# Optimization experiments

Measured on AMD Instinct MI355X. Metric: run time of the kernel, lower is better.

The kernel has to match this reference:

```python
import jax, jax.numpy as jnp
import numpy as np

SIGMA = 1.0
ALPHA = 1.5
EPS = 1e-08
N, D = 8192, 128


def setup_inputs() -> dict:
    key = jax.random.key(0)
    k1, k2 = jax.random.split(key)
    z1 = jax.random.normal(k1, (N, D), dtype=jnp.float32)
    z2 = jax.random.normal(k2, (N, D), dtype=jnp.float32)
    return {"z1": z1, "z2": z2}


def _l2_normalize(x, eps=1e-12):
    # matches F.normalize(x, dim=1): x / max(||x||, eps)
    n = jnp.linalg.norm(x, axis=1, keepdims=True)
    return x / jnp.maximum(n, eps)


def _f_prime(u):
    # KL divergence: f'(u) = log(u + eps) + 1
    return jnp.log(u + EPS) + 1.0


def _f_star(t):
    # KL divergence conjugate: f*(t) = exp(t - 1)
    return jnp.exp(t - 1.0)


def reference(z1, z2):
    z1 = _l2_normalize(z1)
    z2 = _l2_normalize(z2)
    n = z1.shape[0]

    # positive term: ||z1_i - z2_i||^2 per row
    d_pos = jnp.sum((z1 - z2) ** 2, axis=1)                       # (N,)
    g_pos = jnp.exp(-d_pos / (2.0 * SIGMA ** 2))
    s_pos = _f_prime(g_pos)

    # negative term: squared pairwise distances within z1 (N x N)
    sq = jnp.sum(z1 * z1, axis=1)                                  # (N,)
    d2 = sq[:, None] + sq[None, :] - 2.0 * (z1 @ z1.T)             # (N, N)
    d2 = jnp.maximum(d2, 0.0)
    g_neg = jnp.exp(-d2 / (2.0 * SIGMA ** 2))
    s_neg = _f_prime(g_neg)
    star_neg = _f_star(s_neg)

    # masked mean over off-diagonal entries (N*(N-1) of them)
    off_diag = 1.0 - jnp.eye(n, dtype=star_neg.dtype)
    star_mean = jnp.sum(star_neg * off_diag) / (n * (n - 1))

    loss = -jnp.mean(s_pos) + ALPHA * star_mean
    return loss
```

## Files before the change

kernel.cpp:

```cpp
#include <hip/hip_runtime.h>

#define NROWS 8192
#define DIM 128
#define NT 64
#define NBLK 512

typedef _Float16 f16x8 __attribute__((ext_vector_type(8)));
typedef _Float16 f16x2 __attribute__((ext_vector_type(2)));
typedef float f32x16 __attribute__((ext_vector_type(16)));

#define L2E 1.4426950408889634f

#define AS1(p) ((const __attribute__((address_space(1))) void*)(p))
#define AS3(p) ((__attribute__((address_space(3))) void*)(p))

__global__ __launch_bounds__(1024) void fmicl_normalize(
    const float* __restrict__ z1, const float* __restrict__ z2,
    _Float16* __restrict__ zh, float* __restrict__ sposB) {
  const int wid = threadIdx.x >> 6;
  const int lane = threadIdx.x & 63;
  const int row = blockIdx.x * 16 + wid;
  const float2 a = ((const float2*)(z1 + (size_t)row * DIM))[lane];
  const float2 b = ((const float2*)(z2 + (size_t)row * DIM))[lane];
  float s1 = a.x * a.x + a.y * a.y;
  float s2 = b.x * b.x + b.y * b.y;
#pragma unroll
  for (int off = 32; off; off >>= 1) {
    s1 += __shfl_xor(s1, off);
    s2 += __shfl_xor(s2, off);
  }
  const float inv1 = 1.0f / fmaxf(sqrtf(s1), 1e-12f);
  const float inv2 = 1.0f / fmaxf(sqrtf(s2), 1e-12f);
  const float n1x = a.x * inv1, n1y = a.y * inv1;
  const float n2x = b.x * inv2, n2y = b.y * inv2;
  const float dx = n1x - n2x, dy = n1y - n2y;
  float dp = dx * dx + dy * dy;
#pragma unroll
  for (int off = 32; off; off >>= 1) dp += __shfl_xor(dp, off);
  f16x2 h;
  h.x = (_Float16)n1x;
  h.y = (_Float16)n1y;
  *(f16x2*)(zh + (size_t)row * DIM + 2 * lane) = h;
  __shared__ float sposL[16];
  if (lane == 0)
    sposL[wid] = logf(expf(-0.5f * dp) + 1e-8f) + 1.0f;
  __syncthreads();
  if (threadIdx.x == 0) {
    float s = 0.0f;
#pragma unroll
    for (int k = 0; k < 16; ++k) s += sposL[k];
    sposB[blockIdx.x] = s;
  }
}

__device__ __forceinline__ void stageB(const _Float16* __restrict__ zh,
                                       _Float16* buf, int ct, int wid,
                                       int lane) {
  const _Float16* base = zh + ((size_t)ct << 7) * DIM;
#pragma unroll
  for (int it = 0; it < 4; ++it) {
    const int P = it * 8 + wid;
    const int R = P * 4 + (lane >> 4);
    const int cs = (lane & 15) ^ (R & 15);
    __builtin_amdgcn_global_load_lds(AS1(base + (size_t)R * DIM + cs * 8),
                                     AS3(buf + P * 512), 16, 0, 0);
  }
}

__global__ __launch_bounds__(512, 4) void fmicl_pairwise(
    const _Float16* __restrict__ zh, float* __restrict__ pairP) {
  __shared__ _Float16 B0[128 * DIM];
  __shared__ _Float16 B1[128 * DIM];
  __shared__ float wsum[8];

  const int tid = threadIdx.x;
  const int lane = tid & 63;
  const int wid = tid >> 6;
  const int l31 = lane & 31;
  const int lhi = lane >> 5;
  const int m = wid >> 1;
  const int n = wid & 1;

  const int c = (blockIdx.x & 7) * 64 + (blockIdx.x >> 3);
  const int nx = (c + 15) >> 4;
  const int base = 4 * c + nx;
  const int len = 4 + ((c & 15) == 0 ? 1 : 0);

  int rt = (int)(64.5f - sqrtf(64.5f * 64.5f - 2.0f * (float)base));
  if (rt < 0) rt = 0;
  while (rt > 0 && (rt * NT - (rt * (rt - 1)) / 2) > base) --rt;
  while (((rt + 1) * NT - ((rt + 1) * rt) / 2) <= base) ++rt;
  int ctt = rt + (base - (rt * NT - (rt * (rt - 1)) / 2));
  int rtt = rt;

  stageB(zh, B0, ctt, wid, lane);

  uint4 areg[8];
  int cur_rt = -1;
  float gsum = 0.0f;

#pragma unroll 1
  for (int t = 0; t < len; ++t) {
    if (rtt != cur_rt) {
      cur_rt = rtt;
      const uint4* ar =
          (const uint4*)(zh + (size_t)((rtt << 7) + m * 32 + l31) * DIM);
#pragma unroll
      for (int ks = 0; ks < 8; ++ks) areg[ks] = ar[2 * ks + lhi];
    }
    int nrt = rtt, nct = ctt + 1;
    if (nct == NT) { ++nrt; nct = nrt; }
    if (t + 1 < len) {
      stageB(zh, (t & 1) ? B0 : B1, nct, wid, lane);
      asm volatile("s_waitcnt vmcnt(4)" ::: "memory");
    } else {
      asm volatile("s_waitcnt vmcnt(0)" ::: "memory");
    }
    __builtin_amdgcn_s_barrier();
    __builtin_amdgcn_sched_barrier(0);

    const uint4* B4 = (const uint4*)((t & 1) ? B1 : B0);
    const int rb0 = n * 64 + l31;
    const int rb1 = n * 64 + 32 + l31;
    f32x16 acc0 = {}, acc1 = {};
#pragma unroll
    for (int ks = 0; ks < 8; ++ks) {
      const int kg = 2 * ks + lhi;
      const uint4 vb0 = B4[rb0 * 16 + (kg ^ (rb0 & 15))];
      const uint4 vb1 = B4[rb1 * 16 + (kg ^ (rb1 & 15))];
      const f16x8 af = __builtin_bit_cast(f16x8, areg[ks]);
      acc0 = __builtin_amdgcn_mfma_f32_32x32x16_f16(
          af, __builtin_bit_cast(f16x8, vb0), acc0, 0, 0, 0);
      acc1 = __builtin_amdgcn_mfma_f32_32x32x16_f16(
          af, __builtin_bit_cast(f16x8, vb1), acc1, 0, 0, 0);
    }

    float tsum = 0.0f;
    {
      const bool dsub = (rtt == ctt) && (m == 2 * n);
      if (dsub) {
#pragma unroll
        for (int r = 0; r < 16; ++r) {
          const float e = __builtin_amdgcn_exp2f(fmaf(L2E, acc0[r], -L2E));
          const int mloc = (r & 3) + 4 * lhi + 8 * (r >> 2);
          tsum += (mloc != l31) ? e : 0.0f;
        }
      } else {
#pragma unroll
        for (int r = 0; r < 16; ++r)
          tsum += __builtin_amdgcn_exp2f(fmaf(L2E, acc0[r], -L2E));
      }
    }
    {
      const bool dsub = (rtt == ctt) && (m == 2 * n + 1);
      if (dsub) {
#pragma unroll
        for (int r = 0; r < 16; ++r) {
          const float e = __builtin_amdgcn_exp2f(fmaf(L2E, acc1[r], -L2E));
          const int mloc = (r & 3) + 4 * lhi + 8 * (r >> 2);
          tsum += (mloc != l31) ? e : 0.0f;
        }
      } else {
#pragma unroll
        for (int r = 0; r < 16; ++r)
          tsum += __builtin_amdgcn_exp2f(fmaf(L2E, acc1[r], -L2E));
      }
    }
    gsum += (rtt == ctt) ? tsum : (tsum + tsum);

    __builtin_amdgcn_s_barrier();
    rtt = nrt;
    ctt = nct;
  }

#pragma unroll
  for (int off = 32; off; off >>= 1) gsum += __shfl_xor(gsum, off);
  if (lane == 0) wsum[wid] = gsum;
  __syncthreads();
  if (tid == 0) {
    float s = 0.0f;
#pragma unroll
    for (int q = 0; q < 8; ++q) s += wsum[q];
    pairP[c] = s;
  }
}

__global__ void fmicl_reduce(const float* __restrict__ pairP,
                             const float* __restrict__ sposB,
                             float* __restrict__ out) {
  const int t = threadIdx.x;
  double nsum = (t < NBLK) ? (double)pairP[t] : 0.0;
  double psum = (t < 512) ? (double)sposB[t] : 0.0;
#pragma unroll
  for (int off = 32; off; off >>= 1) {
    nsum += __shfl_xor(nsum, off);
    psum += __shfl_xor(psum, off);
  }
  __shared__ double ls[2][16];
  const int lane = t & 63;
  const int wid = t >> 6;
  if (lane == 0) {
    ls[0][wid] = nsum;
    ls[1][wid] = psum;
  }
  __syncthreads();
  if (t == 0) {
    double nn = 0.0, pp = 0.0;
#pragma unroll
    for (int q = 0; q < 16; ++q) {
      nn += ls[0][q];
      pp += ls[1][q];
    }
    const double pos_mean = pp / (double)NROWS;
    const double star_mean = nn / ((double)NROWS * (double)(NROWS - 1)) + 1e-8;
    out[0] = (float)(-pos_mean + 1.5 * star_mean);
  }
}

extern "C" void kernel_launch(void* const* d_in, const int* in_sizes, int n_in,
                              void* d_out, int out_size, void* d_ws,
                              size_t ws_size, hipStream_t stream) {
  const float* z1 = (const float*)d_in[0];
  const float* z2 = (const float*)d_in[1];
  float* out = (float*)d_out;
  char* ws = (char*)d_ws;

  float* pairP = (float*)(ws + 0);
  float* sposB = (float*)(ws + 4096);
  _Float16* zh = (_Float16*)(ws + 6144);

  fmicl_normalize<<<512, 1024, 0, stream>>>(z1, z2, zh, sposB);
  fmicl_pairwise<<<NBLK, 512, 0, stream>>>(zh, pairP);
  fmicl_reduce<<<1, 1024, 0, stream>>>(pairP, sposB, out);
}
```

Before: 30.00 us.

## Prefetch all B tiles into four LDS buffers and remap warps to 2x4 grid

New measurement: 42.60 us. 1.42x slower.

```diff
diff --git a/kernel.cpp b/kernel.cpp
--- a/kernel.cpp
+++ b/kernel.cpp
@@ -67,10 +67,73 @@
   }
 }
 
-__global__ __launch_bounds__(512, 4) void fmicl_pairwise(
+__device__ __forceinline__ void loadA(const _Float16* __restrict__ zh, int rt,
+                                      int mw, int l31, int lhi, uint4* a0,
+                                      uint4* a1) {
+  const uint4* r0 = (const uint4*)(zh + (size_t)((rt << 7) + mw * 64 + l31) * DIM);
+  const uint4* r1 = r0 + 32 * (DIM / 8);
+#pragma unroll
+  for (int ks = 0; ks < 8; ++ks) {
+    a0[ks] = r0[2 * ks + lhi];
+    a1[ks] = r1[2 * ks + lhi];
+  }
+}
+
+__device__ __forceinline__ void computeTile(const _Float16* __restrict__ buf,
+                                            int rtt, int ctt, int mw, int nw,
+                                            int l31, int lhi,
+                                            const uint4* a0, const uint4* a1,
+                                            float& gsum) {
+  const uint4* B4 = (const uint4*)buf;
+  const int rb = nw * 32 + l31;
+  f32x16 acc0 = {}, acc1 = {};
+#pragma unroll
+  for (int ks = 0; ks < 8; ++ks) {
+    const int kg = 2 * ks + lhi;
+    const uint4 vb = B4[rb * 16 + (kg ^ (rb & 15))];
+    const f16x8 bf = __builtin_bit_cast(f16x8, vb);
+    acc0 = __builtin_amdgcn_mfma_f32_32x32x16_f16(
+        __builtin_bit_cast(f16x8, a0[ks]), bf, acc0, 0, 0, 0);
+    acc1 = __builtin_amdgcn_mfma_f32_32x32x16_f16(
+        __builtin_bit_cast(f16x8, a1[ks]), bf, acc1, 0, 0, 0);
+  }
+  float tsum = 0.0f;
+  {
+    const bool dsub = (rtt == ctt) && (nw == 2 * mw);
+    if (dsub) {
+#pragma unroll
+      for (int r = 0; r < 16; ++r) {
+        const float e = __builtin_amdgcn_exp2f(fmaf(L2E, acc0[r], -L2E));
+        const int mloc = (r & 3) + 4 * lhi + 8 * (r >> 2);
+        tsum += (mloc != l31) ? e : 0.0f;
+      }
+    } else {
+#pragma unroll
+      for (int r = 0; r < 16; ++r)
+        tsum += __builtin_amdgcn_exp2f(fmaf(L2E, acc0[r], -L2E));
+    }
+  }
+  {
+    const bool dsub = (rtt == ctt) && (nw == 2 * mw + 1);
+    if (dsub) {
+#pragma unroll
+      for (int r = 0; r < 16; ++r) {
+        const float e = __builtin_amdgcn_exp2f(fmaf(L2E, acc1[r], -L2E));
+        const int mloc = (r & 3) + 4 * lhi + 8 * (r >> 2);
+        tsum += (mloc != l31) ? e : 0.0f;
+      }
+    } else {
+#pragma unroll
+      for (int r = 0; r < 16; ++r)
+        tsum += __builtin_amdgcn_exp2f(fmaf(L2E, acc1[r], -L2E));
+    }
+  }
+  gsum += (rtt == ctt) ? tsum : (tsum + tsum);
+}
+
+__global__ __launch_bounds__(512, 2) void fmicl_pairwise(
     const _Float16* __restrict__ zh, float* __restrict__ pairP) {
-  __shared__ _Float16 B0[128 * DIM];
-  __shared__ _Float16 B1[128 * DIM];
+  __shared__ _Float16 S[4][128 * DIM];
   __shared__ float wsum[8];
 
   const int tid = threadIdx.x;
@@ -78,99 +141,78 @@
   const int wid = tid >> 6;
   const int l31 = lane & 31;
   const int lhi = lane >> 5;
-  const int m = wid >> 1;
-  const int n = wid & 1;
+  const int mw = wid >> 2;
+  const int nw = wid & 3;
 
   const int c = (blockIdx.x & 7) * 64 + (blockIdx.x >> 3);
   const int nx = (c + 15) >> 4;
   const int base = 4 * c + nx;
   const int len = 4 + ((c & 15) == 0 ? 1 : 0);
 
-  int rt = (int)(64.5f - sqrtf(64.5f * 64.5f - 2.0f * (float)base));
-  if (rt < 0) rt = 0;
-  while (rt > 0 && (rt * NT - (rt * (rt - 1)) / 2) > base) --rt;
-  while (((rt + 1) * NT - ((rt + 1) * rt) / 2) <= base) ++rt;
-  int ctt = rt + (base - (rt * NT - (rt * (rt - 1)) / 2));
-  int rtt = rt;
-
-  stageB(zh, B0, ctt, wid, lane);
-
-  uint4 areg[8];
-  int cur_rt = -1;
+  int r0 = (int)(64.5f - sqrtf(64.5f * 64.5f - 2.0f * (float)base));
+  if (r0 < 0) r0 = 0;
+  while (r0 > 0 && (r0 * NT - (r0 * (r0 - 1)) / 2) > base) --r0;
+  while (((r0 + 1) * NT - ((r0 + 1) * r0) / 2) <= base) ++r0;
+  int c0 = r0 + (base - (r0 * NT - (r0 * (r0 - 1)) / 2));
+
+  int r1 = r0, c1 = c0 + 1; if (c1 == NT) { ++r1; c1 = r1; }
+  int r2 = r1, c2 = c1 + 1; if (c2 == NT) { ++r2; c2 = r2; }
+  int r3 = r2, c3 = c2 + 1; if (c3 == NT) { ++r3; c3 = r3; }
+  int r4 = r3, c4 = c3 + 1; if (c4 == NT) { ++r4; c4 = r4; }
+
+  uint4 a0[8], a1[8];
+  loadA(zh, r0, mw, l31, lhi, a0, a1);
+  asm volatile("s_waitcnt vmcnt(0)" ::: "memory");
+
+  stageB(zh, S[0], c0, wid, lane);
+  stageB(zh, S[1], c1, wid, lane);
+  stageB(zh, S[2], c2, wid, lane);
+  stageB(zh, S[3], c3, wid, lane);
+
   float gsum = 0.0f;
 
-#pragma unroll 1
-  for (int t = 0; t < len; ++t) {
-    if (rtt != cur_rt) {
-      cur_rt = rtt;
-      const uint4* ar =
-          (const uint4*)(zh + (size_t)((rtt << 7) + m * 32 + l31) * DIM);
-#pragma unroll
-      for (int ks = 0; ks < 8; ++ks) areg[ks] = ar[2 * ks + lhi];
-    }
-    int nrt = rtt, nct = ctt + 1;
-    if (nct == NT) { ++nrt; nct = nrt; }
-    if (t + 1 < len) {
-      stageB(zh, (t & 1) ? B0 : B1, nct, wid, lane);
-      asm volatile("s_waitcnt vmcnt(4)" ::: "memory");
-    } else {
-      asm volatile("s_waitcnt vmcnt(0)" ::: "memory");
-    }
+  asm volatile("s_waitcnt vmcnt(12)" ::: "memory");
+  __builtin_amdgcn_s_barrier();
+  computeTile(S[0], r0, c0, mw, nw, l31, lhi, a0, a1, gsum);
+  if (len == 5) {
     __builtin_amdgcn_s_barrier();
-    __builtin_amdgcn_sched_barrier(0);
-
-    const uint4* B4 = (const uint4*)((t & 1) ? B1 : B0);
-    const int rb0 = n * 64 + l31;
-    const int rb1 = n * 64 + 32 + l31;
-    f32x16 acc0 = {}, acc1 = {};
-#pragma unroll
-    for (int ks = 0; ks < 8; ++ks) {
-      const int kg = 2 * ks + lhi;
-      const uint4 vb0 = B4[rb0 * 16 + (kg ^ (rb0 & 15))];
-      const uint4 vb1 = B4[rb1 * 16 + (kg ^ (rb1 & 15))];
-      const f16x8 af = __builtin_bit_cast(f16x8, areg[ks]);
-      acc0 = __builtin_amdgcn_mfma_f32_32x32x16_f16(
-          af, __builtin_bit_cast(f16x8, vb0), acc0, 0, 0, 0);
-      acc1 = __builtin_amdgcn_mfma_f32_32x32x16_f16(
-          af, __builtin_bit_cast(f16x8, vb1), acc1, 0, 0, 0);
-    }
-
-    float tsum = 0.0f;
-    {
-      const bool dsub = (rtt == ctt) && (m == 2 * n);
-      if (dsub) {
-#pragma unroll
-        for (int r = 0; r < 16; ++r) {
-          const float e = __builtin_amdgcn_exp2f(fmaf(L2E, acc0[r], -L2E));
-          const int mloc = (r & 3) + 4 * lhi + 8 * (r >> 2);
-          tsum += (mloc != l31) ? e : 0.0f;
-        }
-      } else {
-#pragma unroll
-        for (int r = 0; r < 16; ++r)
-          tsum += __builtin_amdgcn_exp2f(fmaf(L2E, acc0[r], -L2E));
-      }
-    }
-    {
-      const bool dsub = (rtt == ctt) && (m == 2 * n + 1);
-      if (dsub) {
-#pragma unroll
-        for (int r = 0; r < 16; ++r) {
-          const float e = __builtin_amdgcn_exp2f(fmaf(L2E, acc1[r], -L2E));
-          const int mloc = (r & 3) + 4 * lhi + 8 * (r >> 2);
-          tsum += (mloc != l31) ? e : 0.0f;
-        }
-      } else {
-#pragma unroll
-        for (int r = 0; r < 16; ++r)
-          tsum += __builtin_amdgcn_exp2f(fmaf(L2E, acc1[r], -L2E));
-      }
-    }
-    gsum += (rtt == ctt) ? tsum : (tsum + tsum);
-
+    stageB(zh, S[0], c4, wid, lane);
+  }
+  if (r1 != r0) {
+    loadA(zh, r1, mw, l31, lhi, a0, a1);
+    asm volatile("s_waitcnt vmcnt(0)" ::: "memory");
+  }
+  if (len == 5)
+    asm volatile("s_waitcnt vmcnt(12)" ::: "memory");
+  else
+    asm volatile("s_waitcnt vmcnt(8)" ::: "memory");
+  __builtin_amdgcn_s_barrier();
+  computeTile(S[1], r1, c1, mw, nw, l31, lhi, a0, a1, gsum);
+  if (r2 != r1) {
+    loadA(zh, r2, mw, l31, lhi, a0, a1);
+    asm volatile("s_waitcnt vmcnt(0)" ::: "memory");
+  }
+  if (len == 5)
+    asm volatile("s_waitcnt vmcnt(8)" ::: "memory");
+  else
+    asm volatile("s_waitcnt vmcnt(4)" ::: "memory");
+  __builtin_amdgcn_s_barrier();
+  computeTile(S[2], r2, c2, mw, nw, l31, lhi, a0, a1, gsum);
+  if (r3 != r2) {
+    loadA(zh, r3, mw, l31, lhi, a0, a1);
+    asm volatile("s_waitcnt vmcnt(0)" ::: "memory");
+  }
+  if (len == 5)
+    asm volatile("s_waitcnt vmcnt(4)" ::: "memory");
+  else
+    asm volatile("s_waitcnt vmcnt(0)" ::: "memory");
+  __builtin_amdgcn_s_barrier();
+  computeTile(S[3], r3, c3, mw, nw, l31, lhi, a0, a1, gsum);
+  if (len == 5) {
+    if (r4 != r3) loadA(zh, r4, mw, l31, lhi, a0, a1);
+    asm volatile("s_waitcnt vmcnt(0)" ::: "memory");
     __builtin_amdgcn_s_barrier();
-    rtt = nrt;
-    ctt = nct;
+    computeTile(S[0], r4, c4, mw, nw, l31, lhi, a0, a1, gsum);
   }
 
 #pragma unroll
```

## Retile pairwise kernel to 64-row strips with per-wave B slices and finer triangle

Applied to the files above, without the earlier changes.

New measurement: 40.46 us. 1.35x slower.

```diff
diff --git a/kernel.cpp b/kernel.cpp
--- a/kernel.cpp
+++ b/kernel.cpp
@@ -2,8 +2,7 @@
 
 #define NROWS 8192
 #define DIM 128
-#define NT 64
-#define NBLK 512
+#define NBLK 1040
 
 typedef _Float16 f16x8 __attribute__((ext_vector_type(8)));
 typedef _Float16 f16x2 __attribute__((ext_vector_type(2)));
@@ -53,143 +52,127 @@
   }
 }
 
-__device__ __forceinline__ void stageB(const _Float16* __restrict__ zh,
-                                       _Float16* buf, int ct, int wid,
-                                       int lane) {
-  const _Float16* base = zh + ((size_t)ct << 7) * DIM;
-#pragma unroll
-  for (int it = 0; it < 4; ++it) {
-    const int P = it * 8 + wid;
-    const int R = P * 4 + (lane >> 4);
+__device__ __forceinline__ int cfun(int mi) {
+  const int h = mi >> 1;
+  return 64 * mi - (h * h - ((mi & 1) ? 0 : h));
+}
+
+__device__ __forceinline__ void stageSlice(const _Float16* __restrict__ zh,
+                                           _Float16* slice, int gj0,
+                                           int lane) {
+#pragma unroll
+  for (int it = 0; it < 8; ++it) {
+    const int R = it * 4 + (lane >> 4);
     const int cs = (lane & 15) ^ (R & 15);
-    __builtin_amdgcn_global_load_lds(AS1(base + (size_t)R * DIM + cs * 8),
-                                     AS3(buf + P * 512), 16, 0, 0);
-  }
-}
-
-__global__ __launch_bounds__(512, 4) void fmicl_pairwise(
+    __builtin_amdgcn_global_load_lds(
+        AS1(zh + (size_t)(gj0 + R) * DIM + cs * 8), AS3(slice + it * 512), 16,
+        0, 0);
+  }
+}
+
+__device__ __forceinline__ void loadA(const _Float16* __restrict__ zh, int mi,
+                                      int l31, int lhi, uint4* a0, uint4* a1) {
+  const uint4* r0 = (const uint4*)(zh + (size_t)((mi << 6) + l31) * DIM);
+  const uint4* r1 = r0 + 32 * (DIM / 8);
+#pragma unroll
+  for (int ks = 0; ks < 8; ++ks) {
+    a0[ks] = r0[2 * ks + lhi];
+    a1[ks] = r1[2 * ks + lhi];
+  }
+}
+
+__global__ __launch_bounds__(256, 2) void fmicl_pairwise(
     const _Float16* __restrict__ zh, float* __restrict__ pairP) {
-  __shared__ _Float16 B0[128 * DIM];
-  __shared__ _Float16 B1[128 * DIM];
-  __shared__ float wsum[8];
+  __shared__ _Float16 S[2][4][4096];
+  __shared__ float wsum[4];
 
   const int tid = threadIdx.x;
   const int lane = tid & 63;
-  const int wid = tid >> 6;
+  const int nw = tid >> 6;
   const int l31 = lane & 31;
   const int lhi = lane >> 5;
-  const int m = wid >> 1;
-  const int n = wid & 1;
-
-  const int c = (blockIdx.x & 7) * 64 + (blockIdx.x >> 3);
-  const int nx = (c + 15) >> 4;
-  const int base = 4 * c + nx;
-  const int len = 4 + ((c & 15) == 0 ? 1 : 0);
-
-  int rt = (int)(64.5f - sqrtf(64.5f * 64.5f - 2.0f * (float)base));
-  if (rt < 0) rt = 0;
-  while (rt > 0 && (rt * NT - (rt * (rt - 1)) / 2) > base) --rt;
-  while (((rt + 1) * NT - ((rt + 1) * rt) / 2) <= base) ++rt;
-  int ctt = rt + (base - (rt * NT - (rt * (rt - 1)) / 2));
-  int rtt = rt;
-
-  stageB(zh, B0, ctt, wid, lane);
-
-  uint4 areg[8];
-  int cur_rt = -1;
+
+  const int cid = (blockIdx.x & 7) * 130 + (blockIdx.x >> 3);
+  const int base = cid * 4;
+
+  int mi;
+  {
+    const float arg = fmaxf(0.0f, 4096.0f - (float)base);
+    mi = (int)(2.0f * (64.0f - sqrtf(arg)));
+    mi = mi < 0 ? 0 : (mi > 127 ? 127 : mi);
+    while (mi > 0 && cfun(mi) > base) --mi;
+    while (mi < 127 && cfun(mi + 1) <= base) ++mi;
+  }
+  int nj = (mi >> 1) + (base - cfun(mi));
+
+  uint4 a0[8], a1[8];
+  loadA(zh, mi, l31, lhi, a0, a1);
+  stageSlice(zh, S[0][nw], 128 * nj + 32 * nw, lane);
+
   float gsum = 0.0f;
-
 #pragma unroll 1
-  for (int t = 0; t < len; ++t) {
-    if (rtt != cur_rt) {
-      cur_rt = rtt;
-      const uint4* ar =
-          (const uint4*)(zh + (size_t)((rtt << 7) + m * 32 + l31) * DIM);
-#pragma unroll
-      for (int ks = 0; ks < 8; ++ks) areg[ks] = ar[2 * ks + lhi];
-    }
-    int nrt = rtt, nct = ctt + 1;
-    if (nct == NT) { ++nrt; nct = nrt; }
-    if (t + 1 < len) {
-      stageB(zh, (t & 1) ? B0 : B1, nct, wid, lane);
-      asm volatile("s_waitcnt vmcnt(4)" ::: "memory");
+  for (int t = 0; t < 4; ++t) {
+    int mi2 = mi, nj2 = nj + 1;
+    if (nj2 == 64) { ++mi2; nj2 = mi2 >> 1; }
+
+    if (t < 3) {
+      stageSlice(zh, S[(t + 1) & 1][nw], 128 * nj2 + 32 * nw, lane);
+      asm volatile("s_waitcnt vmcnt(8)" ::: "memory");
     } else {
       asm volatile("s_waitcnt vmcnt(0)" ::: "memory");
     }
-    __builtin_amdgcn_s_barrier();
-    __builtin_amdgcn_sched_barrier(0);
-
-    const uint4* B4 = (const uint4*)((t & 1) ? B1 : B0);
-    const int rb0 = n * 64 + l31;
-    const int rb1 = n * 64 + 32 + l31;
+
+    const uint4* B4 = (const uint4*)S[t & 1][nw];
     f32x16 acc0 = {}, acc1 = {};
 #pragma unroll
     for (int ks = 0; ks < 8; ++ks) {
       const int kg = 2 * ks + lhi;
-      const uint4 vb0 = B4[rb0 * 16 + (kg ^ (rb0 & 15))];
-      const uint4 vb1 = B4[rb1 * 16 + (kg ^ (rb1 & 15))];
-      const f16x8 af = __builtin_bit_cast(f16x8, areg[ks]);
+      const uint4 vb = B4[l31 * 16 + (kg ^ (l31 & 15))];
+      const f16x8 bf = __builtin_bit_cast(f16x8, vb);
       acc0 = __builtin_amdgcn_mfma_f32_32x32x16_f16(
-          af, __builtin_bit_cast(f16x8, vb0), acc0, 0, 0, 0);
+          __builtin_bit_cast(f16x8, a0[ks]), bf, acc0, 0, 0, 0);
       acc1 = __builtin_amdgcn_mfma_f32_32x32x16_f16(
-          af, __builtin_bit_cast(f16x8, vb1), acc1, 0, 0, 0);
-    }
-
+          __builtin_bit_cast(f16x8, a1[ks]), bf, acc1, 0, 0, 0);
+    }
+
+    const int jj = 128 * nj + 32 * nw + l31;
     float tsum = 0.0f;
-    {
-      const bool dsub = (rtt == ctt) && (m == 2 * n);
-      if (dsub) {
-#pragma unroll
-        for (int r = 0; r < 16; ++r) {
-          const float e = __builtin_amdgcn_exp2f(fmaf(L2E, acc0[r], -L2E));
-          const int mloc = (r & 3) + 4 * lhi + 8 * (r >> 2);
-          tsum += (mloc != l31) ? e : 0.0f;
-        }
-      } else {
-#pragma unroll
-        for (int r = 0; r < 16; ++r)
-          tsum += __builtin_amdgcn_exp2f(fmaf(L2E, acc0[r], -L2E));
+    if (nj == (mi >> 1)) {
+      const int ii0 = (mi << 6) + 4 * lhi;
+#pragma unroll
+      for (int r = 0; r < 16; ++r) {
+        const float e0 = __builtin_amdgcn_exp2f(fmaf(L2E, acc0[r], -L2E));
+        const float e1 = __builtin_amdgcn_exp2f(fmaf(L2E, acc1[r], -L2E));
+        const int mo = (r & 3) + 8 * (r >> 2);
+        tsum += (jj > ii0 + mo) ? e0 : 0.0f;
+        tsum += (jj > ii0 + 32 + mo) ? e1 : 0.0f;
       }
-    }
-    {
-      const bool dsub = (rtt == ctt) && (m == 2 * n + 1);
-      if (dsub) {
-#pragma unroll
-        for (int r = 0; r < 16; ++r) {
-          const float e = __builtin_amdgcn_exp2f(fmaf(L2E, acc1[r], -L2E));
-          const int mloc = (r & 3) + 4 * lhi + 8 * (r >> 2);
-          tsum += (mloc != l31) ? e : 0.0f;
-        }
-      } else {
-#pragma unroll
-        for (int r = 0; r < 16; ++r)
-          tsum += __builtin_amdgcn_exp2f(fmaf(L2E, acc1[r], -L2E));
+    } else {
+#pragma unroll
+      for (int r = 0; r < 16; ++r) {
+        tsum += __builtin_amdgcn_exp2f(fmaf(L2E, acc0[r], -L2E));
+        tsum += __builtin_amdgcn_exp2f(fmaf(L2E, acc1[r], -L2E));
       }
     }
-    gsum += (rtt == ctt) ? tsum : (tsum + tsum);
-
-    __builtin_amdgcn_s_barrier();
-    rtt = nrt;
-    ctt = nct;
+    gsum += tsum;
+
+    if (t < 3 && mi2 != mi) loadA(zh, mi2, l31, lhi, a0, a1);
+    mi = mi2;
+    nj = nj2;
   }
 
 #pragma unroll
   for (int off = 32; off; off >>= 1) gsum += __shfl_xor(gsum, off);
-  if (lane == 0) wsum[wid] = gsum;
+  if (lane == 0) wsum[nw] = gsum;
   __syncthreads();
-  if (tid == 0) {
-    float s = 0.0f;
-#pragma unroll
-    for (int q = 0; q < 8; ++q) s += wsum[q];
-    pairP[c] = s;
-  }
+  if (tid == 0) pairP[cid] = wsum[0] + wsum[1] + wsum[2] + wsum[3];
 }
 
 __global__ void fmicl_reduce(const float* __restrict__ pairP,
                              const float* __restrict__ sposB,
                              float* __restrict__ out) {
   const int t = threadIdx.x;
-  double nsum = (t < NBLK) ? (double)pairP[t] : 0.0;
+  double nsum = (double)pairP[t] + ((t < NBLK - 1024) ? (double)pairP[t + 1024] : 0.0);
   double psum = (t < 512) ? (double)sposB[t] : 0.0;
 #pragma unroll
   for (int off = 32; off; off >>= 1) {
@@ -212,7 +195,8 @@
       pp += ls[1][q];
     }
     const double pos_mean = pp / (double)NROWS;
-    const double star_mean = nn / ((double)NROWS * (double)(NROWS - 1)) + 1e-8;
+    const double star_mean =
+        2.0 * nn / ((double)NROWS * (double)(NROWS - 1)) + 1e-8;
     out[0] = (float)(-pos_mean + 1.5 * star_mean);
   }
 }
@@ -226,10 +210,10 @@
   char* ws = (char*)d_ws;
 
   float* pairP = (float*)(ws + 0);
-  float* sposB = (float*)(ws + 4096);
-  _Float16* zh = (_Float16*)(ws + 6144);
+  float* sposB = (float*)(ws + 6144);
+  _Float16* zh = (_Float16*)(ws + 8192);
 
   fmicl_normalize<<<512, 1024, 0, stream>>>(z1, z2, zh, sposB);
-  fmicl_pairwise<<<NBLK, 512, 0, stream>>>(zh, pairP);
+  fmicl_pairwise<<<NBLK, 256, 0, stream>>>(zh, pairP);
   fmicl_reduce<<<1, 1024, 0, stream>>>(pairP, sposB, out);
 }
```

## Software-pipeline MFMA tile with previous tile's exp epilogue using double accumulators

Applied to the files above, without the earlier changes.

After: 66.53 us. 2.22x slower.

```diff
diff --git a/kernel.cpp b/kernel.cpp
--- a/kernel.cpp
+++ b/kernel.cpp
@@ -67,6 +67,62 @@
   }
 }
 
+__device__ __forceinline__ void epilogue(const f32x16& acc0,
+                                         const f32x16& acc1, int rtt, int ctt,
+                                         int m, int n, int l31, int lhi,
+                                         float& gsum) {
+  float tsum = 0.0f;
+  {
+    const bool dsub = (rtt == ctt) && (m == 2 * n);
+    if (dsub) {
+#pragma unroll
+      for (int r = 0; r < 16; ++r) {
+        const float e = __builtin_amdgcn_exp2f(fmaf(L2E, acc0[r], -L2E));
+        const int mloc = (r & 3) + 4 * lhi + 8 * (r >> 2);
+        tsum += (mloc != l31) ? e : 0.0f;
+      }
+    } else {
+#pragma unroll
+      for (int r = 0; r < 16; ++r)
+        tsum += __builtin_amdgcn_exp2f(fmaf(L2E, acc0[r], -L2E));
+    }
+  }
+  {
+    const bool dsub = (rtt == ctt) && (m == 2 * n + 1);
+    if (dsub) {
+#pragma unroll
+      for (int r = 0; r < 16; ++r) {
+        const float e = __builtin_amdgcn_exp2f(fmaf(L2E, acc1[r], -L2E));
+        const int mloc = (r & 3) + 4 * lhi + 8 * (r >> 2);
+        tsum += (mloc != l31) ? e : 0.0f;
+      }
+    } else {
+#pragma unroll
+      for (int r = 0; r < 16; ++r)
+        tsum += __builtin_amdgcn_exp2f(fmaf(L2E, acc1[r], -L2E));
+    }
+  }
+  gsum += (rtt == ctt) ? tsum : (tsum + tsum);
+}
+
+__device__ __forceinline__ void mfmaTile(const uint4* B4, int n, int l31,
+                                         int lhi, const uint4* areg,
+                                         f32x16& acc0, f32x16& acc1) {
+  const int rb0 = n * 64 + l31;
+  const int rb1 = n * 64 + 32 + l31;
+#pragma unroll
+  for (int ks = 0; ks < 8; ++ks) {
+    const int kg = 2 * ks + lhi;
+    const uint4 vb0 = B4[rb0 * 16 + (kg ^ (rb0 & 15))];
+    const uint4 vb1 = B4[rb1 * 16 + (kg ^ (rb1 & 15))];
+    const f16x8 af = __builtin_bit_cast(f16x8, areg[ks]);
+    acc0 = __builtin_amdgcn_mfma_f32_32x32x16_f16(
+        af, __builtin_bit_cast(f16x8, vb0), acc0, 0, 0, 0);
+    acc1 = __builtin_amdgcn_mfma_f32_32x32x16_f16(
+        af, __builtin_bit_cast(f16x8, vb1), acc1, 0, 0, 0);
+  }
+}
+
 __global__ __launch_bounds__(512, 4) void fmicl_pairwise(
     const _Float16* __restrict__ zh, float* __restrict__ pairP) {
   __shared__ _Float16 B0[128 * DIM];
@@ -98,6 +154,8 @@
   uint4 areg[8];
   int cur_rt = -1;
   float gsum = 0.0f;
+  f32x16 accA0 = {}, accA1 = {}, accB0 = {}, accB1 = {};
+  int prt = 0, pct = 0;
 
 #pragma unroll 1
   for (int t = 0; t < len; ++t) {
@@ -120,58 +178,28 @@
     __builtin_amdgcn_sched_barrier(0);
 
     const uint4* B4 = (const uint4*)((t & 1) ? B1 : B0);
-    const int rb0 = n * 64 + l31;
-    const int rb1 = n * 64 + 32 + l31;
-    f32x16 acc0 = {}, acc1 = {};
-#pragma unroll
-    for (int ks = 0; ks < 8; ++ks) {
-      const int kg = 2 * ks + lhi;
-      const uint4 vb0 = B4[rb0 * 16 + (kg ^ (rb0 & 15))];
-      const uint4 vb1 = B4[rb1 * 16 + (kg ^ (rb1 & 15))];
-      const f16x8 af = __builtin_bit_cast(f16x8, areg[ks]);
-      acc0 = __builtin_amdgcn_mfma_f32_32x32x16_f16(
-          af, __builtin_bit_cast(f16x8, vb0), acc0, 0, 0, 0);
-      acc1 = __builtin_amdgcn_mfma_f32_32x32x16_f16(
-          af, __builtin_bit_cast(f16x8, vb1), acc1, 0, 0, 0);
-    }
-
-    float tsum = 0.0f;
-    {
-      const bool dsub = (rtt == ctt) && (m == 2 * n);
-      if (dsub) {
-#pragma unroll
-        for (int r = 0; r < 16; ++r) {
-          const float e = __builtin_amdgcn_exp2f(fmaf(L2E, acc0[r], -L2E));
-          const int mloc = (r & 3) + 4 * lhi + 8 * (r >> 2);
-          tsum += (mloc != l31) ? e : 0.0f;
-        }
-      } else {
-#pragma unroll
-        for (int r = 0; r < 16; ++r)
-          tsum += __builtin_amdgcn_exp2f(fmaf(L2E, acc0[r], -L2E));
-      }
-    }
-    {
-      const bool dsub = (rtt == ctt) && (m == 2 * n + 1);
-      if (dsub) {
-#pragma unroll
-        for (int r = 0; r < 16; ++r) {
-          const float e = __builtin_amdgcn_exp2f(fmaf(L2E, acc1[r], -L2E));
-          const int mloc = (r & 3) + 4 * lhi + 8 * (r >> 2);
-          tsum += (mloc != l31) ? e : 0.0f;
-        }
-      } else {
-#pragma unroll
-        for (int r = 0; r < 16; ++r)
-          tsum += __builtin_amdgcn_exp2f(fmaf(L2E, acc1[r], -L2E));
-      }
-    }
-    gsum += (rtt == ctt) ? tsum : (tsum + tsum);
-
-    __builtin_amdgcn_s_barrier();
+    if ((t & 1) == 0) {
+      accA0 = {};
+      accA1 = {};
+      mfmaTile(B4, n, l31, lhi, areg, accA0, accA1);
+      __builtin_amdgcn_s_barrier();
+      if (t > 0) epilogue(accB0, accB1, prt, pct, m, n, l31, lhi, gsum);
+    } else {
+      accB0 = {};
+      accB1 = {};
+      mfmaTile(B4, n, l31, lhi, areg, accB0, accB1);
+      __builtin_amdgcn_s_barrier();
+      epilogue(accA0, accA1, prt, pct, m, n, l31, lhi, gsum);
+    }
+    prt = rtt;
+    pct = ctt;
     rtt = nrt;
     ctt = nct;
   }
+  if ((len & 1) == 0)
+    epilogue(accB0, accB1, prt, pct, m, n, l31, lhi, gsum);
+  else
+    epilogue(accA0, accA1, prt, pct, m, n, l31, lhi, gsum);
 
 #pragma unroll
   for (int off = 32; off; off >>= 1) gsum += __shfl_xor(gsum, off);
```
